# Optimization experiments

Hardware: AMD Instinct MI355X
Metric: run time of the kernel (lower is better)

The kernel has to match this reference:

```python
import jax, jax.numpy as jnp
import numpy as np

N = 100000      # num_nodes
E = 1600000     # num_edges
IN_DIM = 6
EDGE_DIM = 2
H = 5           # heads
C = 5           # out_channels per head (hidden_dim)
D = H * C       # 25, hidden width
L = 3           # num_layers
INV_SQRT_C = np.float32(1.0 / np.sqrt(C))


def setup_inputs() -> dict:
    key = jax.random.key(0)
    ks = jax.random.split(key, 18)
    s = 0.1
    inp = {
        "x": jax.random.normal(ks[0], (N, IN_DIM), dtype=jnp.float32),
        "edge_index": jax.random.randint(ks[1], (2, E), 0, N, dtype=jnp.int64),
        "edge_attr": jax.random.normal(ks[2], (E, EDGE_DIM), dtype=jnp.float32),
        # input projection
        "Wi": jax.random.normal(ks[3], (IN_DIM, D), dtype=jnp.float32) * s,
        "bi": jnp.zeros((D,), dtype=jnp.float32),
        # per-layer TransformerConv params, stacked over layers
        "Wq": jax.random.normal(ks[4], (L, D, D), dtype=jnp.float32) * s,
        "bq": jnp.zeros((L, D), dtype=jnp.float32),
        "Wk": jax.random.normal(ks[5], (L, D, D), dtype=jnp.float32) * s,
        "bk": jnp.zeros((L, D), dtype=jnp.float32),
        "Wv": jax.random.normal(ks[6], (L, D, D), dtype=jnp.float32) * s,
        "bv": jnp.zeros((L, D), dtype=jnp.float32),
        "We": jax.random.normal(ks[7], (L, EDGE_DIM, D), dtype=jnp.float32) * s,  # lin_edge, no bias
        "Wskip": jax.random.normal(ks[8], (L, D, D), dtype=jnp.float32) * s,
        "bskip": jnp.zeros((L, D), dtype=jnp.float32),
        # output head
        "Wo": jax.random.normal(ks[9], (D, 1), dtype=jnp.float32) * s,
        "bo": jnp.zeros((1,), dtype=jnp.float32),
    }
    return inp


def _forward(x, edge_index, edge_attr, Wi, bi, Wq, bq, Wk, bk, Wv, bv, We, Wskip, bskip, Wo, bo):
    src, dst = edge_index[0], edge_index[1]
    h = x @ Wi + bi  # [N, D]
    for l in range(L):
        q = (h @ Wq[l] + bq[l]).reshape(N, H, C)
        k = (h @ Wk[l] + bk[l]).reshape(N, H, C)
        v = (h @ Wv[l] + bv[l]).reshape(N, H, C)
        e = (edge_attr @ We[l]).reshape(E, H, C)  # per-edge projection
        k_j = k[src] + e                           # [E, H, C]
        alpha = jnp.einsum('ehc,ehc->eh', q[dst], k_j) * INV_SQRT_C  # [E, H]
        # scatter-softmax over destination neighborhoods (PyG softmax)
        amax = jax.ops.segment_max(alpha, dst, num_segments=N)       # [N, H]
        ex = jnp.exp(alpha - amax[dst])
        denom = jax.ops.segment_sum(ex, dst, num_segments=N)         # [N, H]
        alpha = ex / (denom[dst] + 1e-16)
        msg = (v[src] + e) * alpha[:, :, None]                       # [E, H, C]
        out = jax.ops.segment_sum(msg, dst, num_segments=N).reshape(N, D)
        h = out + h @ Wskip[l] + bskip[l]          # root_weight skip
    return jax.nn.sigmoid(h @ Wo + bo)             # [N, 1]


def reference(x, edge_index, edge_attr, Wi, bi, Wq, bq, Wk, bk, Wv, bv, We, Wskip, bskip, Wo, bo):
    return _forward(x, edge_index, edge_attr, Wi, bi, Wq, bq, Wk, bk, Wv, bv, We, Wskip, bskip, Wo, bo)
```

## Files before the change

### kernel.cpp

```cpp
#include <hip/hip_runtime.h>
#include <hip/hip_bf16.h>
#include <math.h>

#define NN 100000
#define NE 1600000
#define IN_DIM 6
#define EDGE_DIM 2
#define HH 5
#define CC 5
#define DD 25
#define DS 32
#define INV_SQRT_C 0.4472135954999579f
#define NBUK 200
#define BUKW 500
#define CAP 10000
#define KPB 800
#define CH (NE / KPB)
#define NPB 48
#define NBLK ((NN + NPB - 1) / NPB)


__device__ __forceinline__ unsigned int f2bf(float f) {
    unsigned int u = __float_as_uint(f);
    return (u + 0x7fffu + ((u >> 16) & 1u)) >> 16;
}
__device__ __forceinline__ float bflo(unsigned int u) { return __uint_as_float(u << 16); }
__device__ __forceinline__ float bfhi(unsigned int u) { return __uint_as_float(u & 0xffff0000u); }

__global__ void k_init(int* __restrict__ cursor) {
    int i = threadIdx.x;
    if (i < NBUK) cursor[i] = i * CAP;
}

__global__ __launch_bounds__(256) void k_part(const int* __restrict__ ei,
                                              const float* __restrict__ ea,
                                              int* __restrict__ cursor,
                                              uint2* __restrict__ slab) {
    __shared__ int sdst[CH];
    __shared__ int scnt[NBUK];
    __shared__ int sbase[NBUK];
    __shared__ int swp[NBUK];
    int base = blockIdx.x * CH;
    for (int i = threadIdx.x; i < NBUK; i += 256) scnt[i] = 0;
    __syncthreads();
    for (int i = threadIdx.x; i < CH; i += 256) {
        int dst = ei[NE + base + i];
        sdst[i] = dst;
        atomicAdd(&scnt[dst / BUKW], 1);
    }
    __syncthreads();
    for (int i = threadIdx.x; i < NBUK; i += 256) {
        sbase[i] = atomicAdd(&cursor[i], scnt[i]);
        swp[i] = 0;
    }
    __syncthreads();
    for (int i = threadIdx.x; i < CH; i += 256) {
        int dst = sdst[i];
        int b = dst / BUKW;
        int src = ei[base + i];
        float2 eav = ((const float2*)ea)[base + i];
        int p = sbase[b] + atomicAdd(&swp[b], 1);
        uint2 r;
        r.x = (unsigned)src | ((unsigned)(dst - b * BUKW) << 17);
        r.y = f2bf(eav.x) | (f2bf(eav.y) << 16);
        slab[p] = r;
    }
}

__global__ void k_scanB(const int* __restrict__ cursor, int* __restrict__ bucketOff,
                        int* __restrict__ rowptr) {
    __shared__ int s[256];
    int t = threadIdx.x;
    int v = (t < NBUK) ? (cursor[t] - t * CAP) : 0;
    s[t] = v;
    __syncthreads();
    for (int off = 1; off < 256; off <<= 1) {
        int u = (t >= off) ? s[t - off] : 0;
        __syncthreads();
        s[t] += u;
        __syncthreads();
    }
    if (t < NBUK) bucketOff[t] = s[t] - v;
    if (t == 0) rowptr[NN] = NE;
}

__global__ __launch_bounds__(512) void k_place(const int* __restrict__ cursor,
                                               const uint2* __restrict__ slab,
                                               const int* __restrict__ bucketOff,
                                               int* __restrict__ rowptr,
                                               uint2* __restrict__ csr) {
    __shared__ int hist[BUKW];
    __shared__ int cur[BUKW];
    __shared__ int s[512];
    int b = blockIdx.x;
    int node0 = b * BUKW;
    int begin = b * CAP;
    int cnt = cursor[b] - begin;
    int bOff = bucketOff[b];
    for (int i = threadIdx.x; i < BUKW; i += 512) hist[i] = 0;
    __syncthreads();
    for (int i = threadIdx.x; i < cnt; i += 512) {
        uint2 r = slab[begin + i];
        atomicAdd(&hist[r.x >> 17], 1);
    }
    __syncthreads();
    int t = threadIdx.x;
    int v = (t < BUKW) ? hist[t] : 0;
    s[t] = v;
    __syncthreads();
    for (int off = 1; off < 512; off <<= 1) {
        int u = (t >= off) ? s[t - off] : 0;
        __syncthreads();
        s[t] += u;
        __syncthreads();
    }
    if (t < BUKW) {
        int o = bOff + s[t] - v;
        rowptr[node0 + t] = o;
        cur[t] = o;
    }
    __syncthreads();
    for (int i = threadIdx.x; i < cnt; i += 512) {
        uint2 r = slab[begin + i];
        int dl = (int)(r.x >> 17);
        int p = atomicAdd(&cur[dl], 1);
        uint2 o;
        o.x = r.x & 0x1FFFFu;
        o.y = r.y;
        csr[p] = o;
    }
}

__global__ void k_input_proj(const float* __restrict__ x, const float* __restrict__ Wi,
                             const float* __restrict__ bi, float* __restrict__ h) {
    __shared__ float sW[IN_DIM * DD];
    __shared__ float sb[DD];
    int t = threadIdx.x;
    if (t < IN_DIM * DD) sW[t] = Wi[t];
    if (t < DD) sb[t] = bi[t];
    __syncthreads();
    int tid = blockIdx.x * blockDim.x + t;
    int n = tid / DD, d = tid - n * DD;
    if (n >= NN) return;
    float acc = sb[d];
    const float* xr = x + n * IN_DIM;
#pragma unroll
    for (int i = 0; i < IN_DIM; i++) acc += xr[i] * sW[i * DD + d];
    h[n * DS + d] = acc;
}

__global__ void k_qkv_skip(const float* __restrict__ h,
                           const float* __restrict__ Wq, const float* __restrict__ bq,
                           const float* __restrict__ Wk, const float* __restrict__ bk,
                           const float* __restrict__ Wv, const float* __restrict__ bv,
                           const float* __restrict__ Ws, const float* __restrict__ bs,
                           __hip_bfloat16* __restrict__ q, __hip_bfloat16* __restrict__ kv,
                           float* __restrict__ hout) {
    __shared__ float sWq[DD * DD], sWk[DD * DD], sWv[DD * DD], sWs[DD * DD];
    __shared__ float sb[4 * DD];
    for (int i = threadIdx.x; i < DD * DD; i += blockDim.x) {
        sWq[i] = Wq[i]; sWk[i] = Wk[i]; sWv[i] = Wv[i]; sWs[i] = Ws[i];
    }
    if (threadIdx.x < DD) {
        sb[threadIdx.x]          = bq[threadIdx.x];
        sb[DD + threadIdx.x]     = bk[threadIdx.x];
        sb[2 * DD + threadIdx.x] = bv[threadIdx.x];
        sb[3 * DD + threadIdx.x] = bs[threadIdx.x];
    }
    __syncthreads();
    int tid = blockIdx.x * blockDim.x + threadIdx.x;
    int n = tid / DD, d = tid - n * DD;
    if (n >= NN) return;
    float aq = sb[d], ak = sb[DD + d], av = sb[2 * DD + d], asv = sb[3 * DD + d];
    const float* hr = h + (size_t)n * DS;
#pragma unroll
    for (int i = 0; i < DD; i++) {
        float hv = hr[i];
        aq  += hv * sWq[i * DD + d];
        ak  += hv * sWk[i * DD + d];
        av  += hv * sWv[i * DD + d];
        asv += hv * sWs[i * DD + d];
    }
    int h5 = d / 5, c5 = d - h5 * 5;
    size_t rb = (size_t)n * 64;
    q[rb + 8 * h5 + c5] = __float2bfloat16(aq * INV_SQRT_C);
    kv[rb + 8 * h5 + c5] = __float2bfloat16(ak);
    if (c5 < 3) kv[rb + 8 * h5 + 5 + c5] = __float2bfloat16(av);
    else        kv[rb + 40 + 2 * h5 + (c5 - 3)] = __float2bfloat16(av);
    hout[(size_t)n * DS + d] = asv;
}

__global__ __launch_bounds__(256) void k_edge_fused(
    const int* __restrict__ rowptr, const uint2* __restrict__ csr,
    const float* __restrict__ We, const __hip_bfloat16* __restrict__ q,
    const __hip_bfloat16* __restrict__ kv, float* __restrict__ hout) {
    __shared__ float sWe[EDGE_DIM * DD];
    if (threadIdx.x < EDGE_DIM * DD) sWe[threadIdx.x] = We[threadIdx.x];
    __syncthreads();
    int lane = threadIdx.x & 63;
    int wv   = threadIdx.x >> 6;
    int grp  = lane / 5;
    int h    = lane - grp * 5;
    int node = blockIdx.x * NPB + wv * 12 + grp;
    bool act = (grp < 12) && (node < NN);

    int beg = 0, end = 0;
    float qa0 = 0, qa1 = 0, qa2 = 0, qa3 = 0, qa4 = 0, qwx = 0, qwy = 0;
    if (act) {
        beg = rowptr[node];
        end = rowptr[node + 1];
        uint4 qc = *(const uint4*)(q + (size_t)node * 64 + 8 * h);
        qa0 = bflo(qc.x); qa1 = bfhi(qc.x); qa2 = bflo(qc.y); qa3 = bfhi(qc.y); qa4 = bflo(qc.z);
        const float* wx = &sWe[5 * h];
        const float* wy = &sWe[DD + 5 * h];
        qwx = qa0 * wx[0] + qa1 * wx[1] + qa2 * wx[2] + qa3 * wx[3] + qa4 * wx[4];
        qwy = qa0 * wy[0] + qa1 * wy[1] + qa2 * wy[2] + qa3 * wy[3] + qa4 * wy[4];
    }

    float l = 0.f, Sx = 0.f, Sy = 0.f;
    float a0 = 0.f, a1 = 0.f, a2 = 0.f, a3 = 0.f, a4 = 0.f;

    for (int p = beg; p < end; ++p) {
        uint2 rec = csr[p];
        float eax = bflo(rec.y), eay = bfhi(rec.y);
        const __hip_bfloat16* base = kv + ((size_t)rec.x << 6);
        uint4 A = *(const uint4*)(base + 8 * h);
        unsigned int B = *(const unsigned int*)(base + 40 + 2 * h);
        float k0 = bflo(A.x), k1 = bfhi(A.x), k2 = bflo(A.y), k3 = bfhi(A.y), k4 = bflo(A.z);
        float v0 = bfhi(A.z), v1 = bflo(A.w), v2 = bfhi(A.w), v3 = bflo(B), v4 = bfhi(B);
        float s = qa0 * k0 + qa1 * k1 + qa2 * k2 + qa3 * k3 + qa4 * k4
                + eax * qwx + eay * qwy;
        float cf = __expf(s);
        l  += cf;
        Sx += cf * eax;
        Sy += cf * eay;
        a0 += cf * v0; a1 += cf * v1; a2 += cf * v2; a3 += cf * v3; a4 += cf * v4;
    }

    if (act) {
        float inv = 1.0f / (l + 1e-16f);
        const float* wx = &sWe[5 * h];
        const float* wy = &sWe[DD + 5 * h];
        float* ho = hout + (size_t)node * DS + 5 * h;
        ho[0] += (a0 + Sx * wx[0] + Sy * wy[0]) * inv;
        ho[1] += (a1 + Sx * wx[1] + Sy * wy[1]) * inv;
        ho[2] += (a2 + Sx * wx[2] + Sy * wy[2]) * inv;
        ho[3] += (a3 + Sx * wx[3] + Sy * wy[3]) * inv;
        ho[4] += (a4 + Sx * wx[4] + Sy * wy[4]) * inv;
    }
}

__global__ void k_head(const float* __restrict__ h, const float* __restrict__ Wo,
                       const float* __restrict__ bo, float* __restrict__ out) {
    __shared__ float sW[DD];
    __shared__ float sb0;
    if (threadIdx.x < DD) sW[threadIdx.x] = Wo[threadIdx.x];
    if (threadIdx.x == 0) sb0 = bo[0];
    __syncthreads();
    int n = blockIdx.x * blockDim.x + threadIdx.x;
    if (n >= NN) return;
    float acc = sb0;
    const float* hr = h + (size_t)n * DS;
#pragma unroll
    for (int i = 0; i < DD; i++) acc += hr[i] * sW[i];
    out[n] = 1.0f / (1.0f + __expf(-acc));
}

extern "C" void kernel_launch(void* const* d_in, const int* in_sizes, int n_in,
                              void* d_out, int out_size, void* d_ws, size_t ws_size,
                              hipStream_t stream) {
    const float* x     = (const float*)d_in[0];
    const int*   ei    = (const int*)d_in[1];
    const float* ea    = (const float*)d_in[2];
    const float* Wi    = (const float*)d_in[3];
    const float* bi    = (const float*)d_in[4];
    const float* Wq    = (const float*)d_in[5];
    const float* bq    = (const float*)d_in[6];
    const float* Wk    = (const float*)d_in[7];
    const float* bk    = (const float*)d_in[8];
    const float* Wv    = (const float*)d_in[9];
    const float* bv    = (const float*)d_in[10];
    const float* We    = (const float*)d_in[11];
    const float* Wskip = (const float*)d_in[12];
    const float* bskip = (const float*)d_in[13];
    const float* Wo    = (const float*)d_in[14];
    const float* bo    = (const float*)d_in[15];
    float* out = (float*)d_out;
    (void)in_sizes; (void)n_in; (void)out_size; (void)ws_size;

    char* wsb = (char*)d_ws;
    size_t off = 0;
    auto alloc = [&](size_t bytes) {
        void* p = wsb + off;
        off += (bytes + 127) & ~(size_t)127;
        return p;
    };
    uint2* slab   = (uint2*)alloc((size_t)NBUK * CAP * sizeof(uint2));
    uint2* csr    = (uint2*)alloc((size_t)NE * sizeof(uint2));
    __hip_bfloat16* kvrec = (__hip_bfloat16*)alloc((size_t)NN * 64 * 2);
    __hip_bfloat16* qrec  = (__hip_bfloat16*)alloc((size_t)NN * 64 * 2);
    float* hA     = (float*)alloc((size_t)NN * DS * sizeof(float));
    float* hB     = (float*)alloc((size_t)NN * DS * sizeof(float));
    int*   rowptr = (int*)alloc((size_t)(NN + 1) * sizeof(int));
    int*   cursor = (int*)alloc((size_t)NBUK * sizeof(int));
    int*   bucketOff = (int*)alloc((size_t)NBUK * sizeof(int));

    dim3 blk(256);
    int gN  = (NN + 255) / 256;
    int gND = (NN * DD + 255) / 256;

    k_init<<<1, blk, 0, stream>>>(cursor);
    k_part<<<KPB, blk, 0, stream>>>(ei, ea, cursor, slab);
    k_scanB<<<1, blk, 0, stream>>>(cursor, bucketOff, rowptr);
    k_place<<<NBUK, dim3(512), 0, stream>>>(cursor, slab, bucketOff, rowptr, csr);

    k_input_proj<<<gND, blk, 0, stream>>>(x, Wi, bi, hA);

    float* hc = hA;
    float* hn = hB;
    for (int l = 0; l < 3; l++) {
        k_qkv_skip<<<gND, blk, 0, stream>>>(hc,
                                            Wq + (size_t)l * DD * DD, bq + (size_t)l * DD,
                                            Wk + (size_t)l * DD * DD, bk + (size_t)l * DD,
                                            Wv + (size_t)l * DD * DD, bv + (size_t)l * DD,
                                            Wskip + (size_t)l * DD * DD, bskip + (size_t)l * DD,
                                            qrec, kvrec, hn);
        k_edge_fused<<<NBLK, blk, 0, stream>>>(rowptr, csr,
                                               We + (size_t)l * EDGE_DIM * DD,
                                               qrec, kvrec, hn);
        float* t = hc; hc = hn; hn = t;
    }
    k_head<<<gN, blk, 0, stream>>>(hc, Wo, bo, out);
}
```

Measured before the change: 392.0 us.

## Compact bf16 q/kv records, fuse head into last edge pass, drop scan kernels

Shrinks the per-node kv record from 64 to 50 bf16 values and the q record from 64 to 40, so each gathered neighbour moves fewer bytes. The edge loop now prefetches the next CSR record. The output head is fused into the final edge kernel through a wavefront shuffle reduction. The bucket-offset scan is folded into k_place, and k_init is replaced by a memset, which removes three launches. The kv reads become five 4-byte loads instead of one 16-byte load plus one 4-byte load, and each k_place block now redoes a small reduction over the bucket counts.

```diff
diff --git a/kernel.cpp b/kernel.cpp
--- a/kernel.cpp
+++ b/kernel.cpp
@@ -27,11 +27,6 @@
 __device__ __forceinline__ float bflo(unsigned int u) { return __uint_as_float(u << 16); }
 __device__ __forceinline__ float bfhi(unsigned int u) { return __uint_as_float(u & 0xffff0000u); }
 
-__global__ void k_init(int* __restrict__ cursor) {
-    int i = threadIdx.x;
-    if (i < NBUK) cursor[i] = i * CAP;
-}
-
 __global__ __launch_bounds__(256) void k_part(const int* __restrict__ ei,
                                               const float* __restrict__ ea,
                                               int* __restrict__ cursor,
@@ -50,7 +45,7 @@
     }
     __syncthreads();
     for (int i = threadIdx.x; i < NBUK; i += 256) {
-        sbase[i] = atomicAdd(&cursor[i], scnt[i]);
+        sbase[i] = i * CAP + atomicAdd(&cursor[i], scnt[i]);
         swp[i] = 0;
     }
     __syncthreads();
@@ -67,46 +62,35 @@
     }
 }
 
-__global__ void k_scanB(const int* __restrict__ cursor, int* __restrict__ bucketOff,
-                        int* __restrict__ rowptr) {
-    __shared__ int s[256];
-    int t = threadIdx.x;
-    int v = (t < NBUK) ? (cursor[t] - t * CAP) : 0;
-    s[t] = v;
-    __syncthreads();
-    for (int off = 1; off < 256; off <<= 1) {
-        int u = (t >= off) ? s[t - off] : 0;
-        __syncthreads();
-        s[t] += u;
-        __syncthreads();
-    }
-    if (t < NBUK) bucketOff[t] = s[t] - v;
-    if (t == 0) rowptr[NN] = NE;
-}
-
 __global__ __launch_bounds__(512) void k_place(const int* __restrict__ cursor,
                                                const uint2* __restrict__ slab,
-                                               const int* __restrict__ bucketOff,
                                                int* __restrict__ rowptr,
                                                uint2* __restrict__ csr) {
     __shared__ int hist[BUKW];
     __shared__ int cur[BUKW];
     __shared__ int s[512];
     int b = blockIdx.x;
+    int t = threadIdx.x;
     int node0 = b * BUKW;
     int begin = b * CAP;
-    int cnt = cursor[b] - begin;
-    int bOff = bucketOff[b];
-    for (int i = threadIdx.x; i < BUKW; i += 512) hist[i] = 0;
-    __syncthreads();
-    for (int i = threadIdx.x; i < cnt; i += 512) {
+    int cnt = cursor[b];
+    s[t] = (t < NBUK && t < b) ? cursor[t] : 0;
+    __syncthreads();
+    for (int off = 256; off > 0; off >>= 1) {
+        if (t < off) s[t] += s[t + off];
+        __syncthreads();
+    }
+    int bOff = s[0];
+    __syncthreads();
+    for (int i = t; i < BUKW; i += 512) hist[i] = 0;
+    __syncthreads();
+    for (int i = t; i < cnt; i += 512) {
         uint2 r = slab[begin + i];
         atomicAdd(&hist[r.x >> 17], 1);
     }
     __syncthreads();
-    int t = threadIdx.x;
-    int v = (t < BUKW) ? hist[t] : 0;
-    s[t] = v;
+    int hv = (t < BUKW) ? hist[t] : 0;
+    s[t] = hv;
     __syncthreads();
     for (int off = 1; off < 512; off <<= 1) {
         int u = (t >= off) ? s[t - off] : 0;
@@ -115,12 +99,13 @@
         __syncthreads();
     }
     if (t < BUKW) {
-        int o = bOff + s[t] - v;
+        int o = bOff + s[t] - hv;
         rowptr[node0 + t] = o;
         cur[t] = o;
     }
-    __syncthreads();
-    for (int i = threadIdx.x; i < cnt; i += 512) {
+    if (b == NBUK - 1 && t == 0) rowptr[NN] = NE;
+    __syncthreads();
+    for (int i = t; i < cnt; i += 512) {
         uint2 r = slab[begin + i];
         int dl = (int)(r.x >> 17);
         int p = atomicAdd(&cur[dl], 1);
@@ -181,21 +166,25 @@
         av  += hv * sWv[i * DD + d];
         asv += hv * sWs[i * DD + d];
     }
-    int h5 = d / 5, c5 = d - h5 * 5;
-    size_t rb = (size_t)n * 64;
-    q[rb + 8 * h5 + c5] = __float2bfloat16(aq * INV_SQRT_C);
-    kv[rb + 8 * h5 + c5] = __float2bfloat16(ak);
-    if (c5 < 3) kv[rb + 8 * h5 + 5 + c5] = __float2bfloat16(av);
-    else        kv[rb + 40 + 2 * h5 + (c5 - 3)] = __float2bfloat16(av);
+    int h5 = d / 5, c5 = d - 5 * h5;
+    q[(size_t)n * 40 + 8 * h5 + c5] = __float2bfloat16(aq * INV_SQRT_C);
+    kv[(size_t)n * 50 + 10 * h5 + c5]     = __float2bfloat16(ak);
+    kv[(size_t)n * 50 + 10 * h5 + 5 + c5] = __float2bfloat16(av);
     hout[(size_t)n * DS + d] = asv;
 }
 
 __global__ __launch_bounds__(256) void k_edge_fused(
     const int* __restrict__ rowptr, const uint2* __restrict__ csr,
     const float* __restrict__ We, const __hip_bfloat16* __restrict__ q,
-    const __hip_bfloat16* __restrict__ kv, float* __restrict__ hout) {
+    const __hip_bfloat16* __restrict__ kv, float* __restrict__ hout,
+    int fuse_head, const float* __restrict__ Wo, const float* __restrict__ bo,
+    float* __restrict__ out) {
     __shared__ float sWe[EDGE_DIM * DD];
+    __shared__ float sWo[DD];
+    __shared__ float sbo;
     if (threadIdx.x < EDGE_DIM * DD) sWe[threadIdx.x] = We[threadIdx.x];
+    if (threadIdx.x < DD) sWo[threadIdx.x] = Wo[threadIdx.x];
+    if (threadIdx.x == 0) sbo = bo[0];
     __syncthreads();
     int lane = threadIdx.x & 63;
     int wv   = threadIdx.x >> 6;
@@ -209,7 +198,7 @@
     if (act) {
         beg = rowptr[node];
         end = rowptr[node + 1];
-        uint4 qc = *(const uint4*)(q + (size_t)node * 64 + 8 * h);
+        uint4 qc = *(const uint4*)(q + (size_t)node * 40 + 8 * h);
         qa0 = bflo(qc.x); qa1 = bfhi(qc.x); qa2 = bflo(qc.y); qa3 = bfhi(qc.y); qa4 = bflo(qc.z);
         const float* wx = &sWe[5 * h];
         const float* wy = &sWe[DD + 5 * h];
@@ -220,14 +209,20 @@
     float l = 0.f, Sx = 0.f, Sy = 0.f;
     float a0 = 0.f, a1 = 0.f, a2 = 0.f, a3 = 0.f, a4 = 0.f;
 
-    for (int p = beg; p < end; ++p) {
-        uint2 rec = csr[p];
+    int p = beg;
+    uint2 rec;
+    rec.x = 0; rec.y = 0;
+    if (p < end) rec = csr[p];
+    while (p < end) {
+        int pn = p + 1;
+        uint2 nrec = rec;
+        if (pn < end) nrec = csr[pn];
+        const unsigned int* kb =
+            (const unsigned int*)(kv + (size_t)rec.x * 50 + 10 * h);
+        unsigned int u0 = kb[0], u1 = kb[1], u2 = kb[2], u3 = kb[3], u4 = kb[4];
         float eax = bflo(rec.y), eay = bfhi(rec.y);
-        const __hip_bfloat16* base = kv + ((size_t)rec.x << 6);
-        uint4 A = *(const uint4*)(base + 8 * h);
-        unsigned int B = *(const unsigned int*)(base + 40 + 2 * h);
-        float k0 = bflo(A.x), k1 = bfhi(A.x), k2 = bflo(A.y), k3 = bfhi(A.y), k4 = bflo(A.z);
-        float v0 = bfhi(A.z), v1 = bflo(A.w), v2 = bfhi(A.w), v3 = bflo(B), v4 = bfhi(B);
+        float k0 = bflo(u0), k1 = bfhi(u0), k2 = bflo(u1), k3 = bfhi(u1), k4 = bflo(u2);
+        float v0 = bfhi(u2), v1 = bflo(u3), v2 = bfhi(u3), v3 = bflo(u4), v4 = bfhi(u4);
         float s = qa0 * k0 + qa1 * k1 + qa2 * k2 + qa3 * k3 + qa4 * k4
                 + eax * qwx + eay * qwy;
         float cf = __expf(s);
@@ -235,35 +230,33 @@
         Sx += cf * eax;
         Sy += cf * eay;
         a0 += cf * v0; a1 += cf * v1; a2 += cf * v2; a3 += cf * v3; a4 += cf * v4;
-    }
-
+        rec = nrec;
+        p = pn;
+    }
+
+    float dot = 0.f;
     if (act) {
         float inv = 1.0f / (l + 1e-16f);
         const float* wx = &sWe[5 * h];
         const float* wy = &sWe[DD + 5 * h];
         float* ho = hout + (size_t)node * DS + 5 * h;
-        ho[0] += (a0 + Sx * wx[0] + Sy * wy[0]) * inv;
-        ho[1] += (a1 + Sx * wx[1] + Sy * wy[1]) * inv;
-        ho[2] += (a2 + Sx * wx[2] + Sy * wy[2]) * inv;
-        ho[3] += (a3 + Sx * wx[3] + Sy * wy[3]) * inv;
-        ho[4] += (a4 + Sx * wx[4] + Sy * wy[4]) * inv;
-    }
-}
-
-__global__ void k_head(const float* __restrict__ h, const float* __restrict__ Wo,
-                       const float* __restrict__ bo, float* __restrict__ out) {
-    __shared__ float sW[DD];
-    __shared__ float sb0;
-    if (threadIdx.x < DD) sW[threadIdx.x] = Wo[threadIdx.x];
-    if (threadIdx.x == 0) sb0 = bo[0];
-    __syncthreads();
-    int n = blockIdx.x * blockDim.x + threadIdx.x;
-    if (n >= NN) return;
-    float acc = sb0;
-    const float* hr = h + (size_t)n * DS;
+        float n0 = ho[0] + (a0 + Sx * wx[0] + Sy * wy[0]) * inv;
+        float n1 = ho[1] + (a1 + Sx * wx[1] + Sy * wy[1]) * inv;
+        float n2 = ho[2] + (a2 + Sx * wx[2] + Sy * wy[2]) * inv;
+        float n3 = ho[3] + (a3 + Sx * wx[3] + Sy * wy[3]) * inv;
+        float n4 = ho[4] + (a4 + Sx * wx[4] + Sy * wy[4]) * inv;
+        ho[0] = n0; ho[1] = n1; ho[2] = n2; ho[3] = n3; ho[4] = n4;
+        if (fuse_head) {
+            const float* wo = &sWo[5 * h];
+            dot = n0 * wo[0] + n1 * wo[1] + n2 * wo[2] + n3 * wo[3] + n4 * wo[4];
+        }
+    }
+    if (fuse_head) {
+        float dsum = dot;
 #pragma unroll
-    for (int i = 0; i < DD; i++) acc += hr[i] * sW[i];
-    out[n] = 1.0f / (1.0f + __expf(-acc));
+        for (int k = 1; k < 5; k++) dsum += __shfl(dot, (grp * 5 + k) & 63, 64);
+        if (act && h == 0) out[node] = 1.0f / (1.0f + __expf(-(dsum + sbo)));
+    }
 }
 
 extern "C" void kernel_launch(void* const* d_in, const int* in_sizes, int n_in,
@@ -297,22 +290,19 @@
     };
     uint2* slab   = (uint2*)alloc((size_t)NBUK * CAP * sizeof(uint2));
     uint2* csr    = (uint2*)alloc((size_t)NE * sizeof(uint2));
-    __hip_bfloat16* kvrec = (__hip_bfloat16*)alloc((size_t)NN * 64 * 2);
-    __hip_bfloat16* qrec  = (__hip_bfloat16*)alloc((size_t)NN * 64 * 2);
+    __hip_bfloat16* kvrec = (__hip_bfloat16*)alloc((size_t)NN * 50 * 2);
+    __hip_bfloat16* qrec  = (__hip_bfloat16*)alloc((size_t)NN * 40 * 2);
     float* hA     = (float*)alloc((size_t)NN * DS * sizeof(float));
     float* hB     = (float*)alloc((size_t)NN * DS * sizeof(float));
     int*   rowptr = (int*)alloc((size_t)(NN + 1) * sizeof(int));
     int*   cursor = (int*)alloc((size_t)NBUK * sizeof(int));
-    int*   bucketOff = (int*)alloc((size_t)NBUK * sizeof(int));
 
     dim3 blk(256);
-    int gN  = (NN + 255) / 256;
     int gND = (NN * DD + 255) / 256;
 
-    k_init<<<1, blk, 0, stream>>>(cursor);
+    hipMemsetAsync(cursor, 0, (size_t)NBUK * sizeof(int), stream);
     k_part<<<KPB, blk, 0, stream>>>(ei, ea, cursor, slab);
-    k_scanB<<<1, blk, 0, stream>>>(cursor, bucketOff, rowptr);
-    k_place<<<NBUK, dim3(512), 0, stream>>>(cursor, slab, bucketOff, rowptr, csr);
+    k_place<<<NBUK, dim3(512), 0, stream>>>(cursor, slab, rowptr, csr);
 
     k_input_proj<<<gND, blk, 0, stream>>>(x, Wi, bi, hA);
 
@@ -327,8 +317,8 @@
                                             qrec, kvrec, hn);
         k_edge_fused<<<NBLK, blk, 0, stream>>>(rowptr, csr,
                                                We + (size_t)l * EDGE_DIM * DD,
-                                               qrec, kvrec, hn);
+                                               qrec, kvrec, hn,
+                                               (l == 2) ? 1 : 0, Wo, bo, out);
         float* t = hc; hc = hn; hn = t;
     }
-    k_head<<<gN, blk, 0, stream>>>(hc, Wo, bo, out);
-}
+}
```

After: 381.5 us. 1.03x faster.
